# Kernel optimization log

Hardware: AMD Instinct MI355X
Metric: run time of the kernel (lower is better)

Reference implementation:

```python
import jax, jax.numpy as jnp
import numpy as np
import math

D_MODEL = 1024
N_HEADS = 16
D_K = 64
CHUNK_LEN = 64


def setup_inputs() -> dict:
    key = jax.random.key(0)
    ks = jax.random.split(key, 12)
    hd = N_HEADS * D_K
    s = 0.02
    return {
        'h': jax.random.normal(ks[0], (4, 2048, D_MODEL), jnp.float32),
        'e': jax.random.normal(ks[1], (4, 32, 2, 128, D_MODEL), jnp.float32),
        'Wq': jax.random.normal(ks[2], (D_MODEL, hd), jnp.float32) * s,
        'bq': jnp.zeros((hd,), jnp.float32),
        'Wk': jax.random.normal(ks[3], (D_MODEL, hd), jnp.float32) * s,
        'bk': jnp.zeros((hd,), jnp.float32),
        'Wv': jax.random.normal(ks[4], (D_MODEL, hd), jnp.float32) * s,
        'bv': jnp.zeros((hd,), jnp.float32),
        'Wo': jax.random.normal(ks[5], (hd, D_MODEL), jnp.float32) * s,
        'bo': jnp.zeros((D_MODEL,), jnp.float32),
        'gamma': jnp.ones((D_MODEL,), jnp.float32),
        'beta': jnp.zeros((D_MODEL,), jnp.float32),
    }


def reference(h, e, Wq, bq, Wk, bk, Wv, bv, Wo, bo, gamma, beta):
    b, chunks, neighbors, nlen, d_model = e.shape
    seq_len = h.shape[1]
    scale = 1.0 / math.sqrt(D_K)
    h_res = h
    # shift so chunk i attends to neighbors retrieved for chunk i
    hh = h[:, CHUNK_LEN - 1:]
    # layer norm
    mu = jnp.mean(hh, axis=-1, keepdims=True)
    var = jnp.mean(jnp.square(hh - mu), axis=-1, keepdims=True)
    hh = (hh - mu) / jnp.sqrt(var + 1e-5) * gamma + beta
    # pad to chunks * CHUNK_LEN
    pad = chunks * CHUNK_LEN - hh.shape[1]
    hh = jnp.pad(hh, ((0, 0), (0, pad), (0, 0)))
    hh = hh.reshape(b, chunks, CHUNK_LEN, d_model)
    q = (hh @ Wq + bq).reshape(b, chunks, CHUNK_LEN, N_HEADS, D_K)
    k = (e @ Wk + bk).reshape(b, chunks, neighbors, nlen, N_HEADS, D_K)
    v = (e @ Wv + bv).reshape(b, chunks, neighbors, nlen, N_HEADS, D_K)
    attn = jnp.einsum('bcihd,bcnjhd->bchinj', q, k) * scale  # [b,c,h,i,n,j]
    a_shape = attn.shape
    attn = jax.nn.softmax(attn.reshape(*a_shape[:-2], -1), axis=-1).reshape(a_shape)
    out = jnp.einsum('bchinj,bcnjhd->bcihd', attn, v)
    out = out.reshape(b, chunks * CHUNK_LEN, N_HEADS * D_K)
    out = out @ Wo + bo
    out = jnp.pad(out, ((0, 0), (CHUNK_LEN - 1, 0), (0, 0)))
    return out[:, :seq_len] + h_res
```

## Files before the change

kernel.cpp:

```cpp
#include <hip/hip_runtime.h>
#include <cstdint>
#include <cstddef>


typedef float f32x4 __attribute__((ext_vector_type(4)));
typedef __bf16 bf16x8 __attribute__((ext_vector_type(8)));

static __device__ __forceinline__ ushort f2bf(float f) {
  union { float f; uint32_t u; } x; x.f = f;
  uint32_t r = x.u + 0x7fffu + ((x.u >> 16) & 1u);
  return (ushort)(r >> 16);
}

static __device__ __forceinline__ bf16x8 ld_frag(const ushort* p) {
  union { uint4 u; bf16x8 v; } x;
  x.u = *(const uint4*)p;
  return x.v;
}

static __device__ __forceinline__ void gl2lds16(const ushort* g, ushort* l) {
  __builtin_amdgcn_global_load_lds(
      (const __attribute__((address_space(1))) void*)g,
      (__attribute__((address_space(3))) void*)l,
      16, 0, 0);
}

__global__ __launch_bounds__(256) void transpose_cast4(const float* __restrict__ Wq,
                                                       const float* __restrict__ Wk,
                                                       const float* __restrict__ Wv,
                                                       const float* __restrict__ Wo,
                                                       ushort* __restrict__ WqT,
                                                       ushort* __restrict__ WkvT,
                                                       ushort* __restrict__ WoT) {
  const float* W; ushort* WT;
  switch (blockIdx.z) {
    case 0:  W = Wq; WT = WqT; break;
    case 1:  W = Wk; WT = WkvT; break;
    case 2:  W = Wv; WT = WkvT + (size_t)1024 * 1024; break;
    default: W = Wo; WT = WoT; break;
  }
  __shared__ float tile[64][65];
  const int t = threadIdx.x;
  const int n0 = blockIdx.x * 64, k0 = blockIdx.y * 64;
#pragma unroll
  for (int i = 0; i < 4; ++i) {
    int lid = i * 256 + t;
    int r = lid >> 4, c4 = (lid & 15) * 4;
    float4 v = *(const float4*)&W[(size_t)(k0 + r) * 1024 + n0 + c4];
    tile[r][c4 + 0] = v.x; tile[r][c4 + 1] = v.y;
    tile[r][c4 + 2] = v.z; tile[r][c4 + 3] = v.w;
  }
  __syncthreads();
#pragma unroll
  for (int i = 0; i < 4; ++i) {
    int lid = i * 256 + t;
    int n = lid >> 4, k4 = (lid & 15) * 4;
    ushort4 o;
    o.x = f2bf(tile[k4 + 0][n]); o.y = f2bf(tile[k4 + 1][n]);
    o.z = f2bf(tile[k4 + 2][n]); o.w = f2bf(tile[k4 + 3][n]);
    *(ushort4*)&WT[(size_t)(n0 + n) * 1024 + k0 + k4] = o;
  }
}

__global__ __launch_bounds__(256) void cast_bf16(const float* __restrict__ x,
                                                 ushort* __restrict__ y) {
  const size_t i = ((size_t)blockIdx.x * 256 + threadIdx.x) * 8;
  float4 a = *(const float4*)&x[i];
  float4 b = *(const float4*)&x[i + 4];
  ushort o[8];
  o[0] = f2bf(a.x); o[1] = f2bf(a.y); o[2] = f2bf(a.z); o[3] = f2bf(a.w);
  o[4] = f2bf(b.x); o[5] = f2bf(b.y); o[6] = f2bf(b.z); o[7] = f2bf(b.w);
  *(uint4*)&y[i] = *(const uint4*)o;
}

__global__ __launch_bounds__(256) void ln_kernel(const float* __restrict__ h,
                                                 const float* __restrict__ gamma,
                                                 const float* __restrict__ beta,
                                                 ushort* __restrict__ hh) {
  const int bx = blockIdx.x;
  const int b = bx >> 11, s = bx & 2047;
  const int t = threadIdx.x;
  ushort* orow = hh + (size_t)(b * 2048 + s) * 1024;
  if (s >= 1985) {
    ushort4 z; z.x = 0; z.y = 0; z.z = 0; z.w = 0;
    *(ushort4*)&orow[t * 4] = z;
    return;
  }
  const float* xrow = h + (size_t)(b * 2048 + 63 + s) * 1024;
  float4 x = *(const float4*)&xrow[t * 4];
  float s1 = x.x + x.y + x.z + x.w;
  float s2 = x.x * x.x + x.y * x.y + x.z * x.z + x.w * x.w;
#pragma unroll
  for (int off = 32; off > 0; off >>= 1) {
    s1 += __shfl_xor(s1, off);
    s2 += __shfl_xor(s2, off);
  }
  __shared__ float a1[4], a2[4];
  if ((t & 63) == 0) { a1[t >> 6] = s1; a2[t >> 6] = s2; }
  __syncthreads();
  s1 = a1[0] + a1[1] + a1[2] + a1[3];
  s2 = a2[0] + a2[1] + a2[2] + a2[3];
  const float mu = s1 * (1.0f / 1024.0f);
  const float var = s2 * (1.0f / 1024.0f) - mu * mu;
  const float rstd = rsqrtf(var + 1e-5f);
  float4 g = *(const float4*)&gamma[t * 4];
  float4 be = *(const float4*)&beta[t * 4];
  ushort4 o;
  o.x = f2bf((x.x - mu) * rstd * g.x + be.x);
  o.y = f2bf((x.y - mu) * rstd * g.y + be.y);
  o.z = f2bf((x.z - mu) * rstd * g.z + be.z);
  o.w = f2bf((x.w - mu) * rstd * g.w + be.w);
  *(ushort4*)&orow[t * 4] = o;
}

template <int MODE, int NT>
__global__ __launch_bounds__(256) void gemm_bf16(const ushort* __restrict__ A,
                                                 const ushort* __restrict__ Bt,
                                                 const float* __restrict__ bias,
                                                 const float* __restrict__ bias2,
                                                 ushort* __restrict__ Cbf,
                                                 ushort* __restrict__ Vtg,
                                                 float* __restrict__ Cf,
                                                 const float* __restrict__ resid,
                                                 int mtiles, float scale,
                                                 int mrow_off) {
  __shared__ __align__(16) ushort Alds[2][128 * 32];
  __shared__ __align__(16) ushort Blds[2][128 * 32];
  const int t = threadIdx.x;
  const int lane = t & 63, wave = t >> 6;
  const int quad = lane >> 4, l16 = lane & 15;

  const int L = blockIdx.x;
  const int xcd = L & 7, slot = L >> 3;
  const int nt = slot & (NT - 1);
  const int mt = xcd * (mtiles >> 3) + (slot / NT);
  const int m0 = mt * 128, n0 = nt * 128;

  const int srow = lane >> 2;
  const int scol = (lane & 3) * 8;
  const int c0 = wave * 2;
  const ushort* gA0 = A  + (size_t)(m0 + c0 * 16 + srow) * 1024 + scol;
  const ushort* gA1 = gA0 + 16 * 1024;
  const ushort* gB0 = Bt + (size_t)(n0 + c0 * 16 + srow) * 1024 + scol;
  const ushort* gB1 = gB0 + 16 * 1024;
  ushort* dA0 = &Alds[0][c0 * 512 + lane * 8];
  ushort* dA1 = dA0 + 512;
  ushort* dB0 = &Blds[0][c0 * 512 + lane * 8];
  ushort* dB1 = dB0 + 512;
  const ptrdiff_t SUB = 128 * 32;

  const int wrow = (wave >> 1) * 64, wcol = (wave & 1) * 64;
  const ushort* pA = &Alds[0][(wrow + l16) * 32 + quad * 8];
  const ushort* pB = &Blds[0][(wcol + l16) * 32 + quad * 8];

  f32x4 zero = {0.f, 0.f, 0.f, 0.f};
  f32x4 acc[4][4];
#pragma unroll
  for (int i = 0; i < 4; ++i)
#pragma unroll
    for (int j = 0; j < 4; ++j) acc[i][j] = zero;

  for (int kb = 0; kb < 16; ++kb) {
    const int ko = kb * 64;
    gl2lds16(gA0 + ko, dA0);         gl2lds16(gA1 + ko, dA1);
    gl2lds16(gA0 + ko + 32, dA0 + SUB); gl2lds16(gA1 + ko + 32, dA1 + SUB);
    gl2lds16(gB0 + ko, dB0);         gl2lds16(gB1 + ko, dB1);
    gl2lds16(gB0 + ko + 32, dB0 + SUB); gl2lds16(gB1 + ko + 32, dB1 + SUB);
    __syncthreads();
#pragma unroll
    for (int sub = 0; sub < 2; ++sub) {
      bf16x8 af[4], bfv[4];
#pragma unroll
      for (int i = 0; i < 4; ++i) af[i]  = ld_frag(pA + sub * SUB + i * 512);
#pragma unroll
      for (int j = 0; j < 4; ++j) bfv[j] = ld_frag(pB + sub * SUB + j * 512);
#pragma unroll
      for (int i = 0; i < 4; ++i)
#pragma unroll
        for (int j = 0; j < 4; ++j)
          acc[i][j] = __builtin_amdgcn_mfma_f32_16x16x32_bf16(af[i], bfv[j], acc[i][j], 0, 0, 0);
    }
    __syncthreads();
  }

#pragma unroll
  for (int mi = 0; mi < 4; ++mi)
#pragma unroll
    for (int mj = 0; mj < 4; ++mj) {
      const int cc = n0 + wcol + mj * 16 + l16;
      const int r0 = m0 + wrow + mi * 16 + quad * 4;
      if constexpr (MODE == 0) {
        const float bvb = bias[cc];
#pragma unroll
        for (int rr = 0; rr < 4; ++rr)
          Cbf[(size_t)(r0 + rr) * 1024 + cc] = f2bf((acc[mi][mj][rr] + bvb) * scale);
      } else {
        const float bvb = bias[cc];
#pragma unroll
        for (int rr = 0; rr < 4; ++rr) {
          const int r = r0 + rr;
          const int b = r >> 11, s = r & 2047;
          if (s < 1985) {
            const size_t o = (size_t)(b * 2048 + s + 63) * 1024 + cc;
            Cf[o] = acc[mi][mj][rr] + bvb + resid[o];
          }
        }
      }
    }
}

__global__ __launch_bounds__(512, 2) void gemm_kv256(const ushort* __restrict__ A,
                                                     const ushort* __restrict__ Bt,
                                                     const float* __restrict__ bk_,
                                                     const float* __restrict__ bv_,
                                                     ushort* __restrict__ Kout,
                                                     ushort* __restrict__ Vtg,
                                                     int mrow_off) {
  __shared__ __align__(16) ushort Alds[4 * 8192];
  __shared__ __align__(16) ushort Blds[4 * 8192];

  const int t = threadIdx.x;
  const int lane = t & 63, wave = t >> 6;
  const int wm = wave >> 2, wn = wave & 3;
  const int l16 = lane & 15, quad = lane >> 4;

  const int L = blockIdx.x;
  const int xcd = L & 7, slot = L >> 3;
  const int nt = slot & 7, mt = xcd * 8 + (slot >> 3);
  const int m0 = mt * 256, n0 = nt * 256;

  const int w2 = wave * 2;
  const int srow = lane >> 3;
  const int lanex = (lane & 7) ^ srow;
  const ushort* gA2 = A  + (size_t)(m0 + w2 * 8 + srow) * 1024 + lanex * 8;
  const ushort* gB2 = Bt + (size_t)(n0 + w2 * 8 + srow) * 1024 + lanex * 8;
  ushort* dA2 = Alds + w2 * 512 + lane * 8;
  ushort* dB2 = Blds + w2 * 512 + lane * 8;

  auto stage_a = [&](int ti, int hh) {
    const ushort* g = gA2 + (size_t)hh * 131072 + (size_t)ti * 64;
    ushort* d = dA2 + ((ti & 1) * 2 + hh) * 8192;
    gl2lds16(g, d);
    gl2lds16(g + 8192, d + 512);
  };
  auto stage_b = [&](int ti, int hh) {
    const ushort* g = gB2 + (size_t)hh * 131072 + (size_t)ti * 64;
    ushort* d = dB2 + ((ti & 1) * 2 + hh) * 8192;
    gl2lds16(g, d);
    gl2lds16(g + 8192, d + 512);
  };

  const int b2 = (l16 >> 2) & 1;
  const int qx = (quad ^ (l16 & 3)) << 3;
  const int kof0 = b2 << 5;
  const int kof1 = 32 - kof0;

  f32x4 zero = {0.f, 0.f, 0.f, 0.f};
  f32x4 acc[8][4];
#pragma unroll
  for (int i = 0; i < 8; ++i)
#pragma unroll
    for (int j = 0; j < 4; ++j) acc[i][j] = zero;

  stage_b(0, 0); stage_a(0, 0); stage_b(0, 1); stage_a(0, 1);
  stage_b(1, 0); stage_a(1, 0); stage_b(1, 1);
  asm volatile("s_waitcnt vmcnt(6)" ::: "memory");
  __builtin_amdgcn_s_barrier();

  bf16x8 a[4][2], b01[2][2], b23[2][2];

#pragma unroll 2
  for (int tt = 0; tt < 16; ++tt) {
    const int cur = tt & 1;
    const ushort* pa = Alds + (cur * 2 + wm) * 8192 + l16 * 64 + qx;
    const ushort* pb = Blds + (cur * 2 + (wn >> 1)) * 8192 +
                       ((wn & 1) * 64 + l16) * 64 + qx;

#pragma unroll
    for (int mi = 0; mi < 4; ++mi) {
      a[mi][0] = ld_frag(pa + mi * 1024 + kof0);
      a[mi][1] = ld_frag(pa + mi * 1024 + kof1);
    }
#pragma unroll
    for (int ni = 0; ni < 2; ++ni) {
      b01[ni][0] = ld_frag(pb + ni * 1024 + kof0);
      b01[ni][1] = ld_frag(pb + ni * 1024 + kof1);
    }
    if (tt < 15) stage_a(tt + 1, 1);
    __builtin_amdgcn_s_barrier();
    asm volatile("s_waitcnt lgkmcnt(0)" ::: "memory");
    __builtin_amdgcn_sched_barrier(0);
    __builtin_amdgcn_s_setprio(1);
#pragma unroll
    for (int mi = 0; mi < 4; ++mi)
#pragma unroll
      for (int ni = 0; ni < 2; ++ni) {
        acc[mi][ni] = __builtin_amdgcn_mfma_f32_16x16x32_bf16(a[mi][0], b01[ni][0], acc[mi][ni], 0, 0, 0);
        acc[mi][ni] = __builtin_amdgcn_mfma_f32_16x16x32_bf16(a[mi][1], b01[ni][1], acc[mi][ni], 0, 0, 0);
      }
    __builtin_amdgcn_s_setprio(0);
    __builtin_amdgcn_s_barrier();

#pragma unroll
    for (int ni = 0; ni < 2; ++ni) {
      b23[ni][0] = ld_frag(pb + (ni + 2) * 1024 + kof0);
      b23[ni][1] = ld_frag(pb + (ni + 2) * 1024 + kof1);
    }
    __builtin_amdgcn_s_barrier();
    asm volatile("s_waitcnt lgkmcnt(0)" ::: "memory");
    __builtin_amdgcn_sched_barrier(0);
    __builtin_amdgcn_s_setprio(1);
#pragma unroll
    for (int mi = 0; mi < 4; ++mi)
#pragma unroll
      for (int ni = 0; ni < 2; ++ni) {
        acc[mi][ni + 2] = __builtin_amdgcn_mfma_f32_16x16x32_bf16(a[mi][0], b23[ni][0], acc[mi][ni + 2], 0, 0, 0);
        acc[mi][ni + 2] = __builtin_amdgcn_mfma_f32_16x16x32_bf16(a[mi][1], b23[ni][1], acc[mi][ni + 2], 0, 0, 0);
      }
    __builtin_amdgcn_s_setprio(0);
    __builtin_amdgcn_s_barrier();

#pragma unroll
    for (int mi = 0; mi < 4; ++mi) {
      a[mi][0] = ld_frag(pa + (mi + 4) * 1024 + kof0);
      a[mi][1] = ld_frag(pa + (mi + 4) * 1024 + kof1);
    }
    if (tt < 14) stage_b(tt + 2, 0);
    __builtin_amdgcn_s_barrier();
    asm volatile("s_waitcnt lgkmcnt(0)" ::: "memory");
    __builtin_amdgcn_sched_barrier(0);
    __builtin_amdgcn_s_setprio(1);
#pragma unroll
    for (int mi = 0; mi < 4; ++mi)
#pragma unroll
      for (int ni = 0; ni < 2; ++ni) {
        acc[mi + 4][ni + 2] = __builtin_amdgcn_mfma_f32_16x16x32_bf16(a[mi][0], b23[ni][0], acc[mi + 4][ni + 2], 0, 0, 0);
        acc[mi + 4][ni + 2] = __builtin_amdgcn_mfma_f32_16x16x32_bf16(a[mi][1], b23[ni][1], acc[mi + 4][ni + 2], 0, 0, 0);
      }
    __builtin_amdgcn_s_setprio(0);
    __builtin_amdgcn_s_barrier();

    if (tt < 14) { stage_a(tt + 2, 0); stage_b(tt + 2, 1); }
    __builtin_amdgcn_s_barrier();
    __builtin_amdgcn_s_setprio(1);
#pragma unroll
    for (int mi = 0; mi < 4; ++mi)
#pragma unroll
      for (int ni = 0; ni < 2; ++ni) {
        acc[mi + 4][ni] = __builtin_amdgcn_mfma_f32_16x16x32_bf16(a[mi][0], b01[ni][0], acc[mi + 4][ni], 0, 0, 0);
        acc[mi + 4][ni] = __builtin_amdgcn_mfma_f32_16x16x32_bf16(a[mi][1], b01[ni][1], acc[mi + 4][ni], 0, 0, 0);
      }
    __builtin_amdgcn_s_setprio(0);
    if (tt < 15) {
      if (tt == 14) asm volatile("s_waitcnt vmcnt(0)" ::: "memory");
      else          asm volatile("s_waitcnt vmcnt(6)" ::: "memory");
      __builtin_amdgcn_s_barrier();
    }
  }

  const int rbase = m0 + wm * 128 + quad * 4;
  const int cbase = n0 + wn * 64 + l16;
  if (n0 < 1024) {
#pragma unroll
    for (int mi = 0; mi < 8; ++mi)
#pragma unroll
      for (int ni = 0; ni < 4; ++ni) {
        const int cc = cbase + ni * 16;
        const float bb = bk_[cc];
        const int r0 = rbase + mi * 16;
#pragma unroll
        for (int rr = 0; rr < 4; ++rr)
          Kout[(size_t)(r0 + rr) * 1024 + cc] = f2bf(acc[mi][ni][rr] + bb);
      }
  } else {
#pragma unroll
    for (int mi = 0; mi < 8; ++mi)
#pragma unroll
      for (int ni = 0; ni < 4; ++ni) {
        const int cv = cbase - 1024 + ni * 16;
        const int hh_ = cv >> 6, dd = cv & 63;
        const float bb = bv_[cv];
        const int gr0 = rbase + mi * 16 + mrow_off;
        const int bcl = gr0 >> 8, j0 = gr0 & 255;
        ushort4 o;
        o.x = f2bf(acc[mi][ni][0] + bb);
        o.y = f2bf(acc[mi][ni][1] + bb);
        o.z = f2bf(acc[mi][ni][2] + bb);
        o.w = f2bf(acc[mi][ni][3] + bb);
        *(ushort4*)&Vtg[(size_t)(bcl * 16 + hh_) * 16384 + dd * 256 + j0] = o;
      }
  }
}

__global__ __launch_bounds__(256) void attn_kernel(const ushort* __restrict__ Qb,
                                                   const ushort* __restrict__ Kb,
                                                   const ushort* __restrict__ Vtg,
                                                   ushort* __restrict__ Ob) {
  __shared__ __align__(16) ushort smem[4608 + 18432 + 16896];
  __shared__ float redm[4][64];
  __shared__ float reds[4][64];
  ushort* Qs = smem;
  ushort* Ks = smem + 4608;
  ushort* Vt = smem + 23040;
  ushort* Ps = smem;

  const int t = threadIdx.x;
  const int bx = blockIdx.x;
  const int hd = bx & 15, c = (bx >> 4) & 31, b = bx >> 9;
  const int lane = t & 63, wave = t >> 6;
  const int quad = lane >> 4, l16 = lane & 15;

  const int qrow0 = b * 2048 + c * 64;
  const int kvrow0 = (b * 32 + c) * 256;
  const int colh = hd * 64;
  const ushort* vsrc = Vtg + ((size_t)((b * 32 + c) * 16 + hd)) * 16384;

#pragma unroll
  for (int it = 0; it < 2; ++it) {
    int lid = it * 256 + t;
    int r = lid >> 3, ch = (lid & 7) * 8;
    uint4 v = *(const uint4*)&Qb[(size_t)(qrow0 + r) * 1024 + colh + ch];
    *(uint4*)&Qs[r * 72 + ch] = v;
  }
#pragma unroll
  for (int it = 0; it < 8; ++it) {
    int lid = it * 256 + t;
    int r = lid >> 3, ch = (lid & 7) * 8;
    uint4 v = *(const uint4*)&Kb[(size_t)(kvrow0 + r) * 1024 + colh + ch];
    *(uint4*)&Ks[r * 72 + ch] = v;
  }
#pragma unroll
  for (int it = 0; it < 8; ++it) {
    int lid = it * 256 + t;
    int row = lid >> 5, c8 = (lid & 31) * 8;
    uint4 v = *(const uint4*)&vsrc[row * 256 + c8];
    *(uint4*)&Vt[row * 264 + c8] = v;
  }
  __syncthreads();

  const int jw = wave * 64;
  f32x4 zero = {0.f, 0.f, 0.f, 0.f};
  f32x4 acc[4][4];
#pragma unroll
  for (int i = 0; i < 4; ++i)
#pragma unroll
    for (int j = 0; j < 4; ++j) acc[i][j] = zero;

#pragma unroll
  for (int kb = 0; kb < 2; ++kb) {
    bf16x8 af[4], bfv[4];
#pragma unroll
    for (int mi = 0; mi < 4; ++mi)
      af[mi] = ld_frag(&Qs[(mi * 16 + l16) * 72 + kb * 32 + quad * 8]);
#pragma unroll
    for (int mj = 0; mj < 4; ++mj)
      bfv[mj] = ld_frag(&Ks[(jw + mj * 16 + l16) * 72 + kb * 32 + quad * 8]);
#pragma unroll
    for (int mi = 0; mi < 4; ++mi)
#pragma unroll
      for (int mj = 0; mj < 4; ++mj)
        acc[mi][mj] = __builtin_amdgcn_mfma_f32_16x16x32_bf16(af[mi], bfv[mj], acc[mi][mj], 0, 0, 0);
  }

  float rmax[4][4];
#pragma unroll
  for (int mi = 0; mi < 4; ++mi)
#pragma unroll
    for (int rr = 0; rr < 4; ++rr) {
      float m = fmaxf(fmaxf(acc[mi][0][rr], acc[mi][1][rr]),
                      fmaxf(acc[mi][2][rr], acc[mi][3][rr]));
      m = fmaxf(m, __shfl_xor(m, 1));
      m = fmaxf(m, __shfl_xor(m, 2));
      m = fmaxf(m, __shfl_xor(m, 4));
      m = fmaxf(m, __shfl_xor(m, 8));
      rmax[mi][rr] = m;
    }
  if (l16 == 0) {
#pragma unroll
    for (int mi = 0; mi < 4; ++mi)
#pragma unroll
      for (int rr = 0; rr < 4; ++rr)
        redm[wave][mi * 16 + quad * 4 + rr] = rmax[mi][rr];
  }
  __syncthreads();
  float gmax[4][4];
#pragma unroll
  for (int mi = 0; mi < 4; ++mi)
#pragma unroll
    for (int rr = 0; rr < 4; ++rr) {
      const int row = mi * 16 + quad * 4 + rr;
      gmax[mi][rr] = fmaxf(fmaxf(redm[0][row], redm[1][row]),
                           fmaxf(redm[2][row], redm[3][row]));
    }
  float rsum[4][4];
#pragma unroll
  for (int mi = 0; mi < 4; ++mi)
#pragma unroll
    for (int rr = 0; rr < 4; ++rr) {
      float s = 0.f;
#pragma unroll
      for (int mj = 0; mj < 4; ++mj) {
        float p = exp2f((acc[mi][mj][rr] - gmax[mi][rr]) * 1.4426950408889634f);
        acc[mi][mj][rr] = p;
        s += p;
      }
      s += __shfl_xor(s, 1);
      s += __shfl_xor(s, 2);
      s += __shfl_xor(s, 4);
      s += __shfl_xor(s, 8);
      rsum[mi][rr] = s;
    }
  if (l16 == 0) {
#pragma unroll
    for (int mi = 0; mi < 4; ++mi)
#pragma unroll
      for (int rr = 0; rr < 4; ++rr)
        reds[wave][mi * 16 + quad * 4 + rr] = rsum[mi][rr];
  }
  __syncthreads();
#pragma unroll
  for (int mi = 0; mi < 4; ++mi)
#pragma unroll
    for (int rr = 0; rr < 4; ++rr) {
      const int row = mi * 16 + quad * 4 + rr;
      const float inv = 1.0f / (reds[0][row] + reds[1][row] + reds[2][row] + reds[3][row]);
#pragma unroll
      for (int mj = 0; mj < 4; ++mj)
        Ps[row * 264 + jw + mj * 16 + l16] = f2bf(acc[mi][mj][rr] * inv);
    }
  __syncthreads();

  const int d0 = wave * 16;
  f32x4 acc2[4];
#pragma unroll
  for (int mi = 0; mi < 4; ++mi) acc2[mi] = zero;
#pragma unroll
  for (int kb = 0; kb < 8; ++kb) {
    bf16x8 bfv = ld_frag(&Vt[(d0 + l16) * 264 + kb * 32 + quad * 8]);
#pragma unroll
    for (int mi = 0; mi < 4; ++mi) {
      bf16x8 af = ld_frag(&Ps[(mi * 16 + l16) * 264 + kb * 32 + quad * 8]);
      acc2[mi] = __builtin_amdgcn_mfma_f32_16x16x32_bf16(af, bfv, acc2[mi], 0, 0, 0);
    }
  }
#pragma unroll
  for (int mi = 0; mi < 4; ++mi)
#pragma unroll
    for (int rr = 0; rr < 4; ++rr) {
      const int i = mi * 16 + quad * 4 + rr;
      Ob[(size_t)(qrow0 + i) * 1024 + colh + d0 + l16] = f2bf(acc2[mi][rr]);
    }
}

__global__ __launch_bounds__(256) void head_copy(const float* __restrict__ h,
                                                 float* __restrict__ out) {
  const int idx4 = blockIdx.x * 256 + threadIdx.x;
  const int b = idx4 / 16128;
  const int rem = idx4 - b * 16128;
  const size_t o = (size_t)b * 2048 * 1024 + (size_t)rem * 4;
  *(float4*)&out[o] = *(const float4*)&h[o];
}

extern "C" void kernel_launch(void* const* d_in, const int* in_sizes, int n_in,
                              void* d_out, int out_size, void* d_ws, size_t ws_size,
                              hipStream_t stream) {
  const float* h     = (const float*)d_in[0];
  const float* e     = (const float*)d_in[1];
  const float* Wq    = (const float*)d_in[2];
  const float* bq    = (const float*)d_in[3];
  const float* Wk    = (const float*)d_in[4];
  const float* bk    = (const float*)d_in[5];
  const float* Wv    = (const float*)d_in[6];
  const float* bv    = (const float*)d_in[7];
  const float* Wo    = (const float*)d_in[8];
  const float* bo    = (const float*)d_in[9];
  const float* gamma = (const float*)d_in[10];
  const float* beta  = (const float*)d_in[11];
  float* out = (float*)d_out;

  char* ws = (char*)d_ws;
  ushort* stg  = (ushort*)(ws + ((size_t)0 << 20));
  ushort* WqT  = (ushort*)(ws + ((size_t)32 << 20));
  ushort* WkvT = (ushort*)(ws + ((size_t)34 << 20));
  ushort* WoT  = (ushort*)(ws + ((size_t)38 << 20));
  ushort* Qb   = (ushort*)(ws + ((size_t)40 << 20));
  ushort* Kb   = (ushort*)(ws + ((size_t)56 << 20));
  ushort* VtG  = (ushort*)(ws + ((size_t)120 << 20));

  transpose_cast4<<<dim3(16, 16, 4), 256, 0, stream>>>(Wq, Wk, Wv, Wo, WqT, WkvT, WoT);

  ln_kernel<<<8192, 256, 0, stream>>>(h, gamma, beta, stg);

  gemm_bf16<0, 8><<<512, 256, 0, stream>>>(stg, WqT, bq, nullptr, Qb, nullptr,
                                           nullptr, nullptr, 64, 0.125f, 0);

  for (int half = 0; half < 2; ++half) {
    const size_t roff = (size_t)half * 16384 * 1024;
    cast_bf16<<<8192, 256, 0, stream>>>(e + roff, stg);
    gemm_kv256<<<512, 512, 0, stream>>>(stg, WkvT, bk, bv, Kb + roff,
                                        VtG, half * 16384);
  }

  attn_kernel<<<2048, 256, 0, stream>>>(Qb, Kb, VtG, stg);

  gemm_bf16<1, 8><<<512, 256, 0, stream>>>(stg, WoT, bo, nullptr, nullptr, nullptr,
                                           out, h, 64, 1.0f, 0);
  head_copy<<<252, 256, 0, stream>>>(h, out);
}
```

Before: 524.0 us.

## Fold head copy into output GEMM, reorder GEMM staging, overlap attention loads

The standalone head_copy launch is removed. Its residual copy now runs as 252 extra blocks appended to the output-projection GEMM grid, which saves one kernel launch. The GEMM main loop moves the stage_b(tt+2,1) global-to-LDS prefetch earlier and spreads staging across the compute phases for better overlap. The attention kernel loads Q, K and V into registers up front, delays the V LDS store until after the QK MFMA, and raises wave priority around the MFMA loops, at the cost of more register pressure.

After: 528.6 us. Within noise of the previous version (+0.9%).

```diff
diff --git a/kernel.cpp b/kernel.cpp
--- a/kernel.cpp
+++ b/kernel.cpp
@@ -124,6 +124,16 @@
                                                  const float* __restrict__ resid,
                                                  int mtiles, float scale,
                                                  int mrow_off) {
+  if constexpr (MODE == 1) {
+    if (blockIdx.x >= 512) {
+      const int idx4 = (blockIdx.x - 512) * 256 + threadIdx.x;
+      const int b = idx4 / 16128;
+      const int rem = idx4 - b * 16128;
+      const size_t o = (size_t)b * 2048 * 1024 + (size_t)rem * 4;
+      *(float4*)&Cf[o] = *(const float4*)&resid[o];
+      return;
+    }
+  }
   __shared__ __align__(16) ushort Alds[2][128 * 32];
   __shared__ __align__(16) ushort Blds[2][128 * 32];
   const int t = threadIdx.x;
@@ -306,25 +316,6 @@
       b23[ni][0] = ld_frag(pb + (ni + 2) * 1024 + kof0);
       b23[ni][1] = ld_frag(pb + (ni + 2) * 1024 + kof1);
     }
-    __builtin_amdgcn_s_barrier();
-    asm volatile("s_waitcnt lgkmcnt(0)" ::: "memory");
-    __builtin_amdgcn_sched_barrier(0);
-    __builtin_amdgcn_s_setprio(1);
-#pragma unroll
-    for (int mi = 0; mi < 4; ++mi)
-#pragma unroll
-      for (int ni = 0; ni < 2; ++ni) {
-        acc[mi][ni + 2] = __builtin_amdgcn_mfma_f32_16x16x32_bf16(a[mi][0], b23[ni][0], acc[mi][ni + 2], 0, 0, 0);
-        acc[mi][ni + 2] = __builtin_amdgcn_mfma_f32_16x16x32_bf16(a[mi][1], b23[ni][1], acc[mi][ni + 2], 0, 0, 0);
-      }
-    __builtin_amdgcn_s_setprio(0);
-    __builtin_amdgcn_s_barrier();
-
-#pragma unroll
-    for (int mi = 0; mi < 4; ++mi) {
-      a[mi][0] = ld_frag(pa + (mi + 4) * 1024 + kof0);
-      a[mi][1] = ld_frag(pa + (mi + 4) * 1024 + kof1);
-    }
     if (tt < 14) stage_b(tt + 2, 0);
     __builtin_amdgcn_s_barrier();
     asm volatile("s_waitcnt lgkmcnt(0)" ::: "memory");
@@ -334,13 +325,33 @@
     for (int mi = 0; mi < 4; ++mi)
 #pragma unroll
       for (int ni = 0; ni < 2; ++ni) {
+        acc[mi][ni + 2] = __builtin_amdgcn_mfma_f32_16x16x32_bf16(a[mi][0], b23[ni][0], acc[mi][ni + 2], 0, 0, 0);
+        acc[mi][ni + 2] = __builtin_amdgcn_mfma_f32_16x16x32_bf16(a[mi][1], b23[ni][1], acc[mi][ni + 2], 0, 0, 0);
+      }
+    __builtin_amdgcn_s_setprio(0);
+    __builtin_amdgcn_s_barrier();
+
+#pragma unroll
+    for (int mi = 0; mi < 4; ++mi) {
+      a[mi][0] = ld_frag(pa + (mi + 4) * 1024 + kof0);
+      a[mi][1] = ld_frag(pa + (mi + 4) * 1024 + kof1);
+    }
+    if (tt < 14) stage_b(tt + 2, 1);
+    __builtin_amdgcn_s_barrier();
+    asm volatile("s_waitcnt lgkmcnt(0)" ::: "memory");
+    __builtin_amdgcn_sched_barrier(0);
+    __builtin_amdgcn_s_setprio(1);
+#pragma unroll
+    for (int mi = 0; mi < 4; ++mi)
+#pragma unroll
+      for (int ni = 0; ni < 2; ++ni) {
         acc[mi + 4][ni + 2] = __builtin_amdgcn_mfma_f32_16x16x32_bf16(a[mi][0], b23[ni][0], acc[mi + 4][ni + 2], 0, 0, 0);
         acc[mi + 4][ni + 2] = __builtin_amdgcn_mfma_f32_16x16x32_bf16(a[mi][1], b23[ni][1], acc[mi + 4][ni + 2], 0, 0, 0);
       }
     __builtin_amdgcn_s_setprio(0);
     __builtin_amdgcn_s_barrier();
 
-    if (tt < 14) { stage_a(tt + 2, 0); stage_b(tt + 2, 1); }
+    if (tt < 14) stage_a(tt + 2, 0);
     __builtin_amdgcn_s_barrier();
     __builtin_amdgcn_s_setprio(1);
 #pragma unroll
@@ -415,26 +426,31 @@
   const int colh = hd * 64;
   const ushort* vsrc = Vtg + ((size_t)((b * 32 + c) * 16 + hd)) * 16384;
 
+  uint4 qreg[2], kreg[8], vreg[8];
 #pragma unroll
   for (int it = 0; it < 2; ++it) {
     int lid = it * 256 + t;
-    int r = lid >> 3, ch = (lid & 7) * 8;
-    uint4 v = *(const uint4*)&Qb[(size_t)(qrow0 + r) * 1024 + colh + ch];
-    *(uint4*)&Qs[r * 72 + ch] = v;
+    qreg[it] = *(const uint4*)&Qb[(size_t)(qrow0 + (lid >> 3)) * 1024 + colh + (lid & 7) * 8];
   }
 #pragma unroll
   for (int it = 0; it < 8; ++it) {
     int lid = it * 256 + t;
-    int r = lid >> 3, ch = (lid & 7) * 8;
-    uint4 v = *(const uint4*)&Kb[(size_t)(kvrow0 + r) * 1024 + colh + ch];
-    *(uint4*)&Ks[r * 72 + ch] = v;
+    kreg[it] = *(const uint4*)&Kb[(size_t)(kvrow0 + (lid >> 3)) * 1024 + colh + (lid & 7) * 8];
   }
 #pragma unroll
   for (int it = 0; it < 8; ++it) {
     int lid = it * 256 + t;
-    int row = lid >> 5, c8 = (lid & 31) * 8;
-    uint4 v = *(const uint4*)&vsrc[row * 256 + c8];
-    *(uint4*)&Vt[row * 264 + c8] = v;
+    vreg[it] = *(const uint4*)&vsrc[(lid >> 5) * 256 + (lid & 31) * 8];
+  }
+#pragma unroll
+  for (int it = 0; it < 2; ++it) {
+    int lid = it * 256 + t;
+    *(uint4*)&Qs[(lid >> 3) * 72 + (lid & 7) * 8] = qreg[it];
+  }
+#pragma unroll
+  for (int it = 0; it < 8; ++it) {
+    int lid = it * 256 + t;
+    *(uint4*)&Ks[(lid >> 3) * 72 + (lid & 7) * 8] = kreg[it];
   }
   __syncthreads();
 
@@ -446,6 +462,7 @@
 #pragma unroll
     for (int j = 0; j < 4; ++j) acc[i][j] = zero;
 
+  __builtin_amdgcn_s_setprio(1);
 #pragma unroll
   for (int kb = 0; kb < 2; ++kb) {
     bf16x8 af[4], bfv[4];
@@ -460,6 +477,13 @@
 #pragma unroll
       for (int mj = 0; mj < 4; ++mj)
         acc[mi][mj] = __builtin_amdgcn_mfma_f32_16x16x32_bf16(af[mi], bfv[mj], acc[mi][mj], 0, 0, 0);
+  }
+  __builtin_amdgcn_s_setprio(0);
+
+#pragma unroll
+  for (int it = 0; it < 8; ++it) {
+    int lid = it * 256 + t;
+    *(uint4*)&Vt[(lid >> 5) * 264 + (lid & 31) * 8] = vreg[it];
   }
 
   float rmax[4][4];
@@ -534,6 +558,7 @@
   f32x4 acc2[4];
 #pragma unroll
   for (int mi = 0; mi < 4; ++mi) acc2[mi] = zero;
+  __builtin_amdgcn_s_setprio(1);
 #pragma unroll
   for (int kb = 0; kb < 8; ++kb) {
     bf16x8 bfv = ld_frag(&Vt[(d0 + l16) * 264 + kb * 32 + quad * 8]);
@@ -543,6 +568,7 @@
       acc2[mi] = __builtin_amdgcn_mfma_f32_16x16x32_bf16(af, bfv, acc2[mi], 0, 0, 0);
     }
   }
+  __builtin_amdgcn_s_setprio(0);
 #pragma unroll
   for (int mi = 0; mi < 4; ++mi)
 #pragma unroll
@@ -550,15 +576,6 @@
       const int i = mi * 16 + quad * 4 + rr;
       Ob[(size_t)(qrow0 + i) * 1024 + colh + d0 + l16] = f2bf(acc2[mi][rr]);
     }
-}
-
-__global__ __launch_bounds__(256) void head_copy(const float* __restrict__ h,
-                                                 float* __restrict__ out) {
-  const int idx4 = blockIdx.x * 256 + threadIdx.x;
-  const int b = idx4 / 16128;
-  const int rem = idx4 - b * 16128;
-  const size_t o = (size_t)b * 2048 * 1024 + (size_t)rem * 4;
-  *(float4*)&out[o] = *(const float4*)&h[o];
 }
 
 extern "C" void kernel_launch(void* const* d_in, const int* in_sizes, int n_in,
@@ -603,7 +620,6 @@
 
   attn_kernel<<<2048, 256, 0, stream>>>(Qb, Kb, VtG, stg);
 
-  gemm_bf16<1, 8><<<512, 256, 0, stream>>>(stg, WoT, bo, nullptr, nullptr, nullptr,
+  gemm_bf16<1, 8><<<764, 256, 0, stream>>>(stg, WoT, bo, nullptr, nullptr, nullptr,
                                            out, h, 64, 1.0f, 0);
-  head_copy<<<252, 256, 0, stream>>>(h, out);
-}
+}
```
